# Performance work log

Hardware: AMD Instinct MI355X
Metric: run time of the kernel (lower is better)

The kernel has to match this reference:

```python
import jax, jax.numpy as jnp
import numpy as np

N, E, F, H = 50000, 800000, 64, 4
NEG_SLOPE = 0.2
LN_EPS = 1e-5


def setup_inputs() -> dict:
    key = jax.random.key(0)
    ks = jax.random.split(key, 12)
    h = jax.random.normal(ks[0], (N, F), dtype=jnp.float32)
    src = jax.random.randint(ks[1], (E,), 0, N, dtype=jnp.int32)
    dst = jax.random.randint(ks[2], (E,), 0, N, dtype=jnp.int32)
    s = 1.0 / np.sqrt(F)
    fc_w = jax.random.uniform(ks[3], (F, H * F), jnp.float32, -s, s)
    attn_l = jax.random.normal(ks[4], (H, F), dtype=jnp.float32) * s
    attn_r = jax.random.normal(ks[5], (H, F), dtype=jnp.float32) * s
    gat_bias = jnp.zeros((H * F,), dtype=jnp.float32)
    so = 1.0 / np.sqrt(H * F)
    out_w = jax.random.uniform(ks[6], (H * F, F), jnp.float32, -so, so)
    out_b = jax.random.uniform(ks[7], (F,), jnp.float32, -so, so)
    ln_g = jnp.ones((F,), dtype=jnp.float32)
    ln_b = jnp.zeros((F,), dtype=jnp.float32)
    return {"h": h, "src": src, "dst": dst, "fc_w": fc_w, "attn_l": attn_l,
            "attn_r": attn_r, "gat_bias": gat_bias, "out_w": out_w,
            "out_b": out_b, "ln_g": ln_g, "ln_b": ln_b}


def reference(h, src, dst, fc_w, attn_l, attn_r, gat_bias, out_w, out_b, ln_g, ln_b):
    # --- GATConv (DGL semantics) ---
    feat = (h @ fc_w).reshape(N, H, F)                      # [N,H,F]
    el = jnp.einsum('nhf,hf->nh', feat, attn_l)             # [N,H]
    er = jnp.einsum('nhf,hf->nh', feat, attn_r)             # [N,H]
    e = jax.nn.leaky_relu(el[src] + er[dst], NEG_SLOPE)     # [E,H]
    # edge softmax over incoming edges of each dst node
    m = jax.ops.segment_max(e, dst, num_segments=N)         # [N,H]
    ex = jnp.exp(e - m[dst])                                # [E,H]
    z = jax.ops.segment_sum(ex, dst, num_segments=N)        # [N,H]
    alpha = ex / z[dst]                                     # [E,H]
    msg = feat[src] * alpha[:, :, None]                     # [E,H,F]
    rst = jax.ops.segment_sum(msg, dst, num_segments=N)     # [N,H,F]
    rst = rst + gat_bias.reshape(H, F)
    # --- out linear + layernorm ---
    x = rst.reshape(N, H * F) @ out_w + out_b               # [N,F]
    mu = jnp.mean(x, axis=-1, keepdims=True)
    var = jnp.var(x, axis=-1, keepdims=True)
    return (x - mu) * jax.lax.rsqrt(var + LN_EPS) * ln_g + ln_b
```

## Files before the change

### kernel.cpp

```cpp
#include <hip/hip_runtime.h>

#define NN 50000
#define EE 800000
#define FF 64
#define HH 4
#define HF 256
#define NEG_SLOPE 0.2f
#define LN_EPS 1e-5f
#define WPACK_N (4 * 8 * 64 * 8)
#define WPACKA_N (16 * 2 * 64 * 8)
#define NTILE (NN / 16)
#define TROW 264

typedef __attribute__((ext_vector_type(8))) short s8v;
typedef __attribute__((ext_vector_type(4))) float f4v;

__device__ __forceinline__ unsigned short f32_to_bf16_rne(float x) {
  unsigned int u = __float_as_uint(x);
  unsigned int r = u + 0x7FFFu + ((u >> 16) & 1u);
  return (unsigned short)(r >> 16);
}

__device__ __forceinline__ float readlane_f(float v, int l) {
  return __uint_as_float(
      (unsigned)__builtin_amdgcn_readlane((int)__float_as_uint(v), l));
}

__global__ __launch_bounds__(256) void k_prep(
    const float* __restrict__ fc_w, const float* __restrict__ out_w,
    unsigned short* __restrict__ wpackA, unsigned short* __restrict__ wpack,
    int* __restrict__ cnt) {
  const int idx = blockIdx.x * 256 + threadIdx.x;
  if (idx < WPACKA_N) {
    const int j = idx & 7;
    const int l = (idx >> 3) & 63;
    const int t = (idx >> 9) & 1;
    const int ct = idx >> 10;
    const int k = 32 * t + (l >> 4) * 8 + j;
    const int c = 16 * ct + (l & 15);
    wpackA[idx] = f32_to_bf16_rne(fc_w[k * HF + c]);
  } else if (idx < WPACKA_N + WPACK_N) {
    const int i2 = idx - WPACKA_N;
    const int j = i2 & 7;
    const int l = (i2 >> 3) & 63;
    const int t = (i2 >> 9) & 7;
    const int ct = i2 >> 12;
    const int k = 32 * t + (l >> 4) * 8 + j;
    const int c = 16 * ct + (l & 15);
    wpack[i2] = f32_to_bf16_rne(out_w[k * FF + c]);
  }
  if (idx < NN) cnt[idx] = 0;
}

__global__ __launch_bounds__(256) void k_feat(
    const float* __restrict__ h, const unsigned short* __restrict__ wpackA,
    const float* __restrict__ attn_l, const float* __restrict__ attn_r,
    unsigned short* __restrict__ featb, float* __restrict__ el,
    float* __restrict__ er) {
  __shared__ unsigned short wlds[WPACKA_N];
  {
    const uint4* s = (const uint4*)wpackA;
    uint4* d = (uint4*)wlds;
    for (int i = threadIdx.x; i < 2048; i += 256) d[i] = s[i];
  }
  __syncthreads();
  const int wave = threadIdx.x >> 6;
  const int lane = threadIdx.x & 63;
  const int tile = blockIdx.x * 4 + wave;
  if (tile >= NTILE) return;
  const int n0 = tile * 16;
  const int cl = lane & 15;
  const int quad = lane >> 4;

  float al[16], ar[16];
#pragma unroll
  for (int ct = 0; ct < 16; ++ct) {
    al[ct] = attn_l[16 * ct + cl];
    ar[ct] = attn_r[16 * ct + cl];
  }

  s8v a[2];
#pragma unroll
  for (int t = 0; t < 2; ++t) {
    const float* hp = h + (size_t)(n0 + cl) * FF + 32 * t + quad * 8;
    float hv[8];
    *(float4*)hv = *(const float4*)hp;
    *(float4*)(hv + 4) = *(const float4*)(hp + 4);
    s8v av;
#pragma unroll
    for (int i = 0; i < 8; ++i) av[i] = (short)f32_to_bf16_rne(hv[i]);
    a[t] = av;
  }

  f4v acc[16];
#pragma unroll
  for (int ct = 0; ct < 16; ++ct) {
    f4v z = {0.f, 0.f, 0.f, 0.f};
    acc[ct] = z;
#pragma unroll
    for (int t = 0; t < 2; ++t) {
      const s8v b = *(const s8v*)(wlds + ((ct * 2 + t) * 64 + lane) * 8);
      acc[ct] = __builtin_amdgcn_mfma_f32_16x16x32_bf16(a[t], b, acc[ct], 0, 0, 0);
    }
  }

#pragma unroll
  for (int r = 0; r < 4; ++r) {
    const int n = n0 + quad * 4 + r;
    float pl[4] = {0.f, 0.f, 0.f, 0.f};
    float pr[4] = {0.f, 0.f, 0.f, 0.f};
#pragma unroll
    for (int g = 0; g < 4; ++g) {
      const float x0 = acc[g][r];
      const float x1 = acc[g + 4][r];
      const float x2 = acc[g + 8][r];
      const float x3 = acc[g + 12][r];
      uint2 pk;
      pk.x = (unsigned)f32_to_bf16_rne(x0) | ((unsigned)f32_to_bf16_rne(x1) << 16);
      pk.y = (unsigned)f32_to_bf16_rne(x2) | ((unsigned)f32_to_bf16_rne(x3) << 16);
      *(uint2*)(featb + (size_t)n * HF + (16 * g + cl) * 4) = pk;
      pl[0] = fmaf(x0, al[g], pl[0]);      pr[0] = fmaf(x0, ar[g], pr[0]);
      pl[1] = fmaf(x1, al[g + 4], pl[1]);  pr[1] = fmaf(x1, ar[g + 4], pr[1]);
      pl[2] = fmaf(x2, al[g + 8], pl[2]);  pr[2] = fmaf(x2, ar[g + 8], pr[2]);
      pl[3] = fmaf(x3, al[g + 12], pl[3]); pr[3] = fmaf(x3, ar[g + 12], pr[3]);
    }
#pragma unroll
    for (int off = 1; off < 16; off <<= 1) {
#pragma unroll
      for (int hh = 0; hh < 4; ++hh) {
        pl[hh] += __shfl_xor(pl[hh], off, 64);
        pr[hh] += __shfl_xor(pr[hh], off, 64);
      }
    }
    if (cl == 0) {
      *(float4*)(el + (size_t)n * 4) = make_float4(pl[0], pl[1], pl[2], pl[3]);
      *(float4*)(er + (size_t)n * 4) = make_float4(pr[0], pr[1], pr[2], pr[3]);
    }
  }
}

__global__ void k_scatter(const int* __restrict__ src,
                          const int* __restrict__ dst,
                          int* __restrict__ cnt, int* __restrict__ colp) {
  int e = blockIdx.x * blockDim.x + threadIdx.x;
  if (e < EE) {
    const int d = dst[e];
    const int pos = atomicAdd(&cnt[d], 1);
    if (pos < 64) colp[(d << 6) | pos] = src[e];
  }
}

__global__ __launch_bounds__(256) void k_gather_out(
    const unsigned short* __restrict__ featb, const float* __restrict__ el,
    const float* __restrict__ er, const int* __restrict__ cnt,
    const int* __restrict__ colp, const float* __restrict__ gat_bias,
    const unsigned short* __restrict__ wpack, const float* __restrict__ out_b,
    const float* __restrict__ ln_g, const float* __restrict__ ln_b,
    float* __restrict__ out) {
  __shared__ unsigned short tile[16][TROW];
  const int wave = threadIdx.x >> 6;
  const int lane = threadIdx.x & 63;
  const int n0 = blockIdx.x * 16;
  const float gb0 = gat_bias[lane], gb1 = gat_bias[64 + lane];
  const float gb2 = gat_bias[128 + lane], gb3 = gat_bias[192 + lane];
  const unsigned short* fb = featb + lane * HH;

#pragma unroll
  for (int r = 0; r < 4; ++r) {
    const int row = wave * 4 + r;
    const int n = n0 + row;
    const int m = cnt[n];
    const float4 erv = *(const float4*)(er + (size_t)n * 4);
    float a0 = 0.f, a1 = 0.f, a2 = 0.f, a3 = 0.f;
    float z0 = 0.f, z1 = 0.f, z2 = 0.f, z3 = 0.f;
    float w0 = 0.f, w1 = 0.f, w2 = 0.f, w3 = 0.f;
    int s = 0;
    if (lane < m) {
      s = colp[(n << 6) | lane];
      const float4 elv = *(const float4*)(el + (size_t)s * 4);
      float e0 = elv.x + erv.x, e1 = elv.y + erv.y;
      float e2 = elv.z + erv.z, e3 = elv.w + erv.w;
      e0 = e0 > 0.f ? e0 : NEG_SLOPE * e0;
      e1 = e1 > 0.f ? e1 : NEG_SLOPE * e1;
      e2 = e2 > 0.f ? e2 : NEG_SLOPE * e2;
      e3 = e3 > 0.f ? e3 : NEG_SLOPE * e3;
      w0 = __expf(e0); w1 = __expf(e1);
      w2 = __expf(e2); w3 = __expf(e3);
    }
    for (int e = 0; e < m; e += 8) {
#pragma unroll
      for (int j = 0; j < 8; ++j) {
        const int le = e + j;
        const int se = __builtin_amdgcn_readlane(s, le);
        const float we0 = readlane_f(w0, le);
        const float we1 = readlane_f(w1, le);
        const float we2 = readlane_f(w2, le);
        const float we3 = readlane_f(w3, le);
        const uint2 d = *(const uint2*)(fb + (size_t)se * HF);
        z0 += we0; z1 += we1; z2 += we2; z3 += we3;
        a0 = fmaf(we0, __uint_as_float(d.x << 16), a0);
        a1 = fmaf(we1, __uint_as_float(d.x & 0xFFFF0000u), a1);
        a2 = fmaf(we2, __uint_as_float(d.y << 16), a2);
        a3 = fmaf(we3, __uint_as_float(d.y & 0xFFFF0000u), a3);
      }
    }
    tile[row][lane]       = f32_to_bf16_rne((z0 > 0.f ? a0 / z0 : 0.f) + gb0);
    tile[row][64 + lane]  = f32_to_bf16_rne((z1 > 0.f ? a1 / z1 : 0.f) + gb1);
    tile[row][128 + lane] = f32_to_bf16_rne((z2 > 0.f ? a2 / z2 : 0.f) + gb2);
    tile[row][192 + lane] = f32_to_bf16_rne((z3 > 0.f ? a3 / z3 : 0.f) + gb3);
  }
  __syncthreads();
  if (wave != 0) return;

  const int cl = lane & 15;
  const int quad = lane >> 4;
  s8v a[8];
#pragma unroll
  for (int t = 0; t < 8; ++t)
    a[t] = *(const s8v*)(&tile[cl][32 * t + quad * 8]);

  f4v acc[4];
#pragma unroll
  for (int ct = 0; ct < 4; ++ct) {
    f4v z = {0.f, 0.f, 0.f, 0.f};
    acc[ct] = z;
#pragma unroll
    for (int t = 0; t < 8; ++t) {
      const s8v b = *(const s8v*)(wpack + ((ct * 8 + t) * 64 + lane) * 8);
      acc[ct] = __builtin_amdgcn_mfma_f32_16x16x32_bf16(a[t], b, acc[ct], 0, 0, 0);
    }
  }

  float x[4][4];
  float s1[4], s2[4];
#pragma unroll
  for (int r = 0; r < 4; ++r) { s1[r] = 0.f; s2[r] = 0.f; }
#pragma unroll
  for (int ct = 0; ct < 4; ++ct) {
    const float ob = out_b[16 * ct + cl];
#pragma unroll
    for (int r = 0; r < 4; ++r) {
      const float v = acc[ct][r] + ob;
      x[ct][r] = v;
      s1[r] += v;
      s2[r] += v * v;
    }
  }
#pragma unroll
  for (int r = 0; r < 4; ++r) {
#pragma unroll
    for (int off = 1; off < 16; off <<= 1) {
      s1[r] += __shfl_xor(s1[r], off, 64);
      s2[r] += __shfl_xor(s2[r], off, 64);
    }
  }
#pragma unroll
  for (int r = 0; r < 4; ++r) {
    const float mu = s1[r] * (1.f / 64.f);
    const float var = s2[r] * (1.f / 64.f) - mu * mu;
    const float inv = rsqrtf(var + LN_EPS);
    const int row = n0 + quad * 4 + r;
#pragma unroll
    for (int ct = 0; ct < 4; ++ct) {
      const int c = 16 * ct + cl;
      out[(size_t)row * FF + c] = (x[ct][r] - mu) * inv * ln_g[c] + ln_b[c];
    }
  }
}

extern "C" void kernel_launch(void* const* d_in, const int* in_sizes, int n_in,
                              void* d_out, int out_size, void* d_ws,
                              size_t ws_size, hipStream_t stream) {
  const float* h_in   = (const float*)d_in[0];
  const int*   src    = (const int*)d_in[1];
  const int*   dst    = (const int*)d_in[2];
  const float* fc_w   = (const float*)d_in[3];
  const float* attn_l = (const float*)d_in[4];
  const float* attn_r = (const float*)d_in[5];
  const float* gbias  = (const float*)d_in[6];
  const float* out_w  = (const float*)d_in[7];
  const float* out_b  = (const float*)d_in[8];
  const float* ln_g   = (const float*)d_in[9];
  const float* ln_b   = (const float*)d_in[10];
  float* out = (float*)d_out;

  char* p = (char*)d_ws;
  auto alloc = [&](size_t bytes) {
    char* q = p;
    p += (bytes + 255) & ~(size_t)255;
    return q;
  };
  unsigned short* featb  = (unsigned short*)alloc((size_t)NN * HF * 2);
  unsigned short* wpack  = (unsigned short*)alloc((size_t)WPACK_N * 2);
  unsigned short* wpackA = (unsigned short*)alloc((size_t)WPACKA_N * 2);
  float* el      = (float*)alloc((size_t)NN * HH * 4);
  float* er      = (float*)alloc((size_t)NN * HH * 4);
  int*   cnt     = (int*)alloc((size_t)NN * 4);
  int*   colp    = (int*)alloc((size_t)NN * 64 * 4);

  k_prep<<<256, 256, 0, stream>>>(fc_w, out_w, wpackA, wpack, cnt);
  k_feat<<<(NTILE + 3) / 4, 256, 0, stream>>>(h_in, wpackA, attn_l, attn_r,
                                              featb, el, er);
  k_scatter<<<(EE + 255) / 256, 256, 0, stream>>>(src, dst, cnt, colp);
  k_gather_out<<<NTILE, 256, 0, stream>>>(featb, el, er, cnt, colp, gbias,
                                          wpack, out_b, ln_g, ln_b, out);
}
```

Baseline: 210.2 us.

## Interleave gathers across four rows and split output GEMM over all waves

Each wave now computes edge weights for its four destination rows up front and gets the softmax denominators with a wave-wide shuffle reduction. It then issues the feature gathers for all four rows in one batch per 8-edge step, which raises memory-level parallelism over the old row-by-row loop. The output projection and LayerNorm are split so that each of the four waves computes one 16-column tile, with the row statistics combined through shared memory. The cost is more registers held for the batched gathers, which may lower occupancy, plus an extra barrier.

```diff
diff --git a/kernel.cpp b/kernel.cpp
--- a/kernel.cpp
+++ b/kernel.cpp
@@ -158,24 +158,24 @@
     const float* __restrict__ ln_g, const float* __restrict__ ln_b,
     float* __restrict__ out) {
   __shared__ unsigned short tile[16][TROW];
+  __shared__ float part[4][16][2];
   const int wave = threadIdx.x >> 6;
   const int lane = threadIdx.x & 63;
   const int n0 = blockIdx.x * 16;
-  const float gb0 = gat_bias[lane], gb1 = gat_bias[64 + lane];
-  const float gb2 = gat_bias[128 + lane], gb3 = gat_bias[192 + lane];
   const unsigned short* fb = featb + lane * HH;
 
-#pragma unroll
-  for (int r = 0; r < 4; ++r) {
-    const int row = wave * 4 + r;
-    const int n = n0 + row;
-    const int m = cnt[n];
+  int mr[4], sv[4];
+  float wa[4], wb[4], wc[4], wd[4];
+#pragma unroll
+  for (int r = 0; r < 4; ++r) {
+    const int n = n0 + wave * 4 + r;
+    int m = cnt[n];
+    m = m > 64 ? 64 : m;
+    mr[r] = __builtin_amdgcn_readfirstlane(m);
     const float4 erv = *(const float4*)(er + (size_t)n * 4);
-    float a0 = 0.f, a1 = 0.f, a2 = 0.f, a3 = 0.f;
-    float z0 = 0.f, z1 = 0.f, z2 = 0.f, z3 = 0.f;
-    float w0 = 0.f, w1 = 0.f, w2 = 0.f, w3 = 0.f;
     int s = 0;
-    if (lane < m) {
+    float x0 = 0.f, x1 = 0.f, x2 = 0.f, x3 = 0.f;
+    if (lane < mr[r]) {
       s = colp[(n << 6) | lane];
       const float4 elv = *(const float4*)(el + (size_t)s * 4);
       float e0 = elv.x + erv.x, e1 = elv.y + erv.y;
@@ -184,87 +184,122 @@
       e1 = e1 > 0.f ? e1 : NEG_SLOPE * e1;
       e2 = e2 > 0.f ? e2 : NEG_SLOPE * e2;
       e3 = e3 > 0.f ? e3 : NEG_SLOPE * e3;
-      w0 = __expf(e0); w1 = __expf(e1);
-      w2 = __expf(e2); w3 = __expf(e3);
-    }
-    for (int e = 0; e < m; e += 8) {
-#pragma unroll
-      for (int j = 0; j < 8; ++j) {
-        const int le = e + j;
-        const int se = __builtin_amdgcn_readlane(s, le);
-        const float we0 = readlane_f(w0, le);
-        const float we1 = readlane_f(w1, le);
-        const float we2 = readlane_f(w2, le);
-        const float we3 = readlane_f(w3, le);
-        const uint2 d = *(const uint2*)(fb + (size_t)se * HF);
-        z0 += we0; z1 += we1; z2 += we2; z3 += we3;
-        a0 = fmaf(we0, __uint_as_float(d.x << 16), a0);
-        a1 = fmaf(we1, __uint_as_float(d.x & 0xFFFF0000u), a1);
-        a2 = fmaf(we2, __uint_as_float(d.y << 16), a2);
-        a3 = fmaf(we3, __uint_as_float(d.y & 0xFFFF0000u), a3);
+      x0 = __expf(e0); x1 = __expf(e1);
+      x2 = __expf(e2); x3 = __expf(e3);
+    }
+    sv[r] = s;
+    wa[r] = x0; wb[r] = x1; wc[r] = x2; wd[r] = x3;
+  }
+
+  float za[4], zb[4], zc[4], zd[4];
+#pragma unroll
+  for (int r = 0; r < 4; ++r) {
+    float z0 = wa[r], z1 = wb[r], z2 = wc[r], z3 = wd[r];
+#pragma unroll
+    for (int off = 1; off < 64; off <<= 1) {
+      z0 += __shfl_xor(z0, off, 64);
+      z1 += __shfl_xor(z1, off, 64);
+      z2 += __shfl_xor(z2, off, 64);
+      z3 += __shfl_xor(z3, off, 64);
+    }
+    za[r] = z0; zb[r] = z1; zc[r] = z2; zd[r] = z3;
+  }
+
+  float a0[4] = {0.f, 0.f, 0.f, 0.f};
+  float a1[4] = {0.f, 0.f, 0.f, 0.f};
+  float a2[4] = {0.f, 0.f, 0.f, 0.f};
+  float a3[4] = {0.f, 0.f, 0.f, 0.f};
+  int mmax = mr[0] > mr[1] ? mr[0] : mr[1];
+  mmax = mmax > mr[2] ? mmax : mr[2];
+  mmax = mmax > mr[3] ? mmax : mr[3];
+
+  for (int e = 0; e < mmax; e += 8) {
+    uint2 d[4][8];
+#pragma unroll
+    for (int r = 0; r < 4; ++r) {
+      if (e < mr[r]) {
+#pragma unroll
+        for (int j = 0; j < 8; ++j) {
+          const int se = __builtin_amdgcn_readlane(sv[r], e + j);
+          d[r][j] = *(const uint2*)(fb + (size_t)se * HF);
+        }
       }
     }
-    tile[row][lane]       = f32_to_bf16_rne((z0 > 0.f ? a0 / z0 : 0.f) + gb0);
-    tile[row][64 + lane]  = f32_to_bf16_rne((z1 > 0.f ? a1 / z1 : 0.f) + gb1);
-    tile[row][128 + lane] = f32_to_bf16_rne((z2 > 0.f ? a2 / z2 : 0.f) + gb2);
-    tile[row][192 + lane] = f32_to_bf16_rne((z3 > 0.f ? a3 / z3 : 0.f) + gb3);
+#pragma unroll
+    for (int r = 0; r < 4; ++r) {
+      if (e < mr[r]) {
+#pragma unroll
+        for (int j = 0; j < 8; ++j) {
+          const int le = e + j;
+          const float we0 = readlane_f(wa[r], le);
+          const float we1 = readlane_f(wb[r], le);
+          const float we2 = readlane_f(wc[r], le);
+          const float we3 = readlane_f(wd[r], le);
+          a0[r] = fmaf(we0, __uint_as_float(d[r][j].x << 16), a0[r]);
+          a1[r] = fmaf(we1, __uint_as_float(d[r][j].x & 0xFFFF0000u), a1[r]);
+          a2[r] = fmaf(we2, __uint_as_float(d[r][j].y << 16), a2[r]);
+          a3[r] = fmaf(we3, __uint_as_float(d[r][j].y & 0xFFFF0000u), a3[r]);
+        }
+      }
+    }
+  }
+
+  const float gb0 = gat_bias[lane], gb1 = gat_bias[64 + lane];
+  const float gb2 = gat_bias[128 + lane], gb3 = gat_bias[192 + lane];
+#pragma unroll
+  for (int r = 0; r < 4; ++r) {
+    const int row = wave * 4 + r;
+    tile[row][lane]       = f32_to_bf16_rne((za[r] > 0.f ? a0[r] / za[r] : 0.f) + gb0);
+    tile[row][64 + lane]  = f32_to_bf16_rne((zb[r] > 0.f ? a1[r] / zb[r] : 0.f) + gb1);
+    tile[row][128 + lane] = f32_to_bf16_rne((zc[r] > 0.f ? a2[r] / zc[r] : 0.f) + gb2);
+    tile[row][192 + lane] = f32_to_bf16_rne((zd[r] > 0.f ? a3[r] / zd[r] : 0.f) + gb3);
   }
   __syncthreads();
-  if (wave != 0) return;
 
   const int cl = lane & 15;
   const int quad = lane >> 4;
-  s8v a[8];
+  s8v afr[8];
 #pragma unroll
   for (int t = 0; t < 8; ++t)
-    a[t] = *(const s8v*)(&tile[cl][32 * t + quad * 8]);
-
-  f4v acc[4];
-#pragma unroll
-  for (int ct = 0; ct < 4; ++ct) {
-    f4v z = {0.f, 0.f, 0.f, 0.f};
-    acc[ct] = z;
-#pragma unroll
-    for (int t = 0; t < 8; ++t) {
-      const s8v b = *(const s8v*)(wpack + ((ct * 8 + t) * 64 + lane) * 8);
-      acc[ct] = __builtin_amdgcn_mfma_f32_16x16x32_bf16(a[t], b, acc[ct], 0, 0, 0);
-    }
-  }
-
-  float x[4][4];
-  float s1[4], s2[4];
-#pragma unroll
-  for (int r = 0; r < 4; ++r) { s1[r] = 0.f; s2[r] = 0.f; }
-#pragma unroll
-  for (int ct = 0; ct < 4; ++ct) {
-    const float ob = out_b[16 * ct + cl];
-#pragma unroll
-    for (int r = 0; r < 4; ++r) {
-      const float v = acc[ct][r] + ob;
-      x[ct][r] = v;
-      s1[r] += v;
-      s2[r] += v * v;
-    }
-  }
-#pragma unroll
-  for (int r = 0; r < 4; ++r) {
+    afr[t] = *(const s8v*)(&tile[cl][32 * t + quad * 8]);
+
+  f4v acc = {0.f, 0.f, 0.f, 0.f};
+#pragma unroll
+  for (int t = 0; t < 8; ++t) {
+    const s8v b = *(const s8v*)(wpack + ((wave * 8 + t) * 64 + lane) * 8);
+    acc = __builtin_amdgcn_mfma_f32_16x16x32_bf16(afr[t], b, acc, 0, 0, 0);
+  }
+
+  const float ob = out_b[16 * wave + cl];
+  float xv[4];
+#pragma unroll
+  for (int r = 0; r < 4; ++r) {
+    const float v = acc[r] + ob;
+    xv[r] = v;
+    float p1 = v, p2 = v * v;
 #pragma unroll
     for (int off = 1; off < 16; off <<= 1) {
-      s1[r] += __shfl_xor(s1[r], off, 64);
-      s2[r] += __shfl_xor(s2[r], off, 64);
-    }
-  }
-#pragma unroll
-  for (int r = 0; r < 4; ++r) {
-    const float mu = s1[r] * (1.f / 64.f);
-    const float var = s2[r] * (1.f / 64.f) - mu * mu;
+      p1 += __shfl_xor(p1, off, 64);
+      p2 += __shfl_xor(p2, off, 64);
+    }
+    if (cl == 0) {
+      part[wave][quad * 4 + r][0] = p1;
+      part[wave][quad * 4 + r][1] = p2;
+    }
+  }
+  __syncthreads();
+#pragma unroll
+  for (int r = 0; r < 4; ++r) {
+    const int row = quad * 4 + r;
+    const float t1 = part[0][row][0] + part[1][row][0] +
+                     part[2][row][0] + part[3][row][0];
+    const float t2 = part[0][row][1] + part[1][row][1] +
+                     part[2][row][1] + part[3][row][1];
+    const float mu = t1 * (1.f / 64.f);
+    const float var = t2 * (1.f / 64.f) - mu * mu;
     const float inv = rsqrtf(var + LN_EPS);
-    const int row = n0 + quad * 4 + r;
-#pragma unroll
-    for (int ct = 0; ct < 4; ++ct) {
-      const int c = 16 * ct + cl;
-      out[(size_t)row * FF + c] = (x[ct][r] - mu) * inv * ln_g[c] + ln_b[c];
-    }
+    const int c = 16 * wave + cl;
+    out[(size_t)(n0 + row) * FF + c] = (xv[r] - mu) * inv * ln_g[c] + ln_b[c];
   }
 }
 
```

After: 236.4 us. 12.5% more time.

## Fuse edge scatter and feature projection into one horizontally-fused kernel

Applied to the files above, without the earlier changes.

Merges the CSR-bucket scatter kernel and the feature-projection MFMA kernel into a single launch, with block ranges split between the two independent jobs so they can run concurrently and one launch gap disappears. The feature path also stops staging the packed weights in LDS and reads B fragments straight from global memory (L2/L1-cached), so there is no block-level sync. The trade-off is more global loads per wave for the weights and a possible loss of occupancy balance, since the scatter blocks are light and the feat blocks are heavy.

```diff
diff --git a/kernel.cpp b/kernel.cpp
--- a/kernel.cpp
+++ b/kernel.cpp
@@ -11,6 +11,8 @@
 #define WPACKA_N (16 * 2 * 64 * 8)
 #define NTILE (NN / 16)
 #define TROW 264
+#define FEAT_BLOCKS ((NTILE + 3) / 4)
+#define SCAT_BLOCKS ((EE + 255) / 256)
 
 typedef __attribute__((ext_vector_type(8))) short s8v;
 typedef __attribute__((ext_vector_type(4))) float f4v;
@@ -52,21 +54,27 @@
   if (idx < NN) cnt[idx] = 0;
 }
 
-__global__ __launch_bounds__(256) void k_feat(
+__global__ __launch_bounds__(256) void k_feat_scatter(
     const float* __restrict__ h, const unsigned short* __restrict__ wpackA,
     const float* __restrict__ attn_l, const float* __restrict__ attn_r,
     unsigned short* __restrict__ featb, float* __restrict__ el,
-    float* __restrict__ er) {
-  __shared__ unsigned short wlds[WPACKA_N];
-  {
-    const uint4* s = (const uint4*)wpackA;
-    uint4* d = (uint4*)wlds;
-    for (int i = threadIdx.x; i < 2048; i += 256) d[i] = s[i];
-  }
-  __syncthreads();
+    float* __restrict__ er, const int* __restrict__ src,
+    const int* __restrict__ dst, int* __restrict__ cnt,
+    int* __restrict__ colp) {
+  const int bid = blockIdx.x;
+  if (bid < SCAT_BLOCKS) {
+    const int e = bid * 256 + threadIdx.x;
+    if (e < EE) {
+      const int sv = src[e];
+      const int d = dst[e];
+      const int pos = atomicAdd(&cnt[d], 1);
+      if (pos < 64) colp[(d << 6) | pos] = sv;
+    }
+    return;
+  }
   const int wave = threadIdx.x >> 6;
   const int lane = threadIdx.x & 63;
-  const int tile = blockIdx.x * 4 + wave;
+  const int tile = (bid - SCAT_BLOCKS) * 4 + wave;
   if (tile >= NTILE) return;
   const int n0 = tile * 16;
   const int cl = lane & 15;
@@ -99,7 +107,7 @@
     acc[ct] = z;
 #pragma unroll
     for (int t = 0; t < 2; ++t) {
-      const s8v b = *(const s8v*)(wlds + ((ct * 2 + t) * 64 + lane) * 8);
+      const s8v b = *(const s8v*)(wpackA + ((ct * 2 + t) * 64 + lane) * 8);
       acc[ct] = __builtin_amdgcn_mfma_f32_16x16x32_bf16(a[t], b, acc[ct], 0, 0, 0);
     }
   }
@@ -136,17 +144,6 @@
       *(float4*)(el + (size_t)n * 4) = make_float4(pl[0], pl[1], pl[2], pl[3]);
       *(float4*)(er + (size_t)n * 4) = make_float4(pr[0], pr[1], pr[2], pr[3]);
     }
-  }
-}
-
-__global__ void k_scatter(const int* __restrict__ src,
-                          const int* __restrict__ dst,
-                          int* __restrict__ cnt, int* __restrict__ colp) {
-  int e = blockIdx.x * blockDim.x + threadIdx.x;
-  if (e < EE) {
-    const int d = dst[e];
-    const int pos = atomicAdd(&cnt[d], 1);
-    if (pos < 64) colp[(d << 6) | pos] = src[e];
   }
 }
 
@@ -299,9 +296,8 @@
   int*   colp    = (int*)alloc((size_t)NN * 64 * 4);
 
   k_prep<<<256, 256, 0, stream>>>(fc_w, out_w, wpackA, wpack, cnt);
-  k_feat<<<(NTILE + 3) / 4, 256, 0, stream>>>(h_in, wpackA, attn_l, attn_r,
-                                              featb, el, er);
-  k_scatter<<<(EE + 255) / 256, 256, 0, stream>>>(src, dst, cnt, colp);
+  k_feat_scatter<<<SCAT_BLOCKS + FEAT_BLOCKS, 256, 0, stream>>>(
+      h_in, wpackA, attn_l, attn_r, featb, el, er, src, dst, cnt, colp);
   k_gather_out<<<NTILE, 256, 0, stream>>>(featb, el, er, cnt, colp, gbias,
                                           wpack, out_b, ln_g, ln_b, out);
 }
```

Result: slower. 226.1 us (+7.6%).

## Fold fc_w into out_w and attention vectors; aggregate raw h instead of feat

Applied to the files above, without the earlier changes.

Uses linearity to precompute fc_w·out_w per head, fc_w·attn_l/attn_r, and gat_bias·out_w+out_b in the prep kernel. The per-node projection to the 256-wide feat tensor is removed: el/er come from dot products of h with the folded vectors, and the gather aggregates 64-wide bf16 h rows with per-head weights. This cuts gather traffic from 512 B to 128 B per edge and eliminates the feat GEMM. The attention weights are normalised once up front instead of dividing after accumulation. Rounding changes because the folded weights are quantised to bf16 and h is rounded to bf16 before aggregation.

```diff
diff --git a/kernel.cpp b/kernel.cpp
--- a/kernel.cpp
+++ b/kernel.cpp
@@ -8,7 +8,6 @@
 #define NEG_SLOPE 0.2f
 #define LN_EPS 1e-5f
 #define WPACK_N (4 * 8 * 64 * 8)
-#define WPACKA_N (16 * 2 * 64 * 8)
 #define NTILE (NN / 16)
 #define TROW 264
 
@@ -28,113 +27,73 @@
 
 __global__ __launch_bounds__(256) void k_prep(
     const float* __restrict__ fc_w, const float* __restrict__ out_w,
-    unsigned short* __restrict__ wpackA, unsigned short* __restrict__ wpack,
+    const float* __restrict__ attn_l, const float* __restrict__ attn_r,
+    const float* __restrict__ gat_bias, const float* __restrict__ out_b,
+    unsigned short* __restrict__ wpack, float* __restrict__ alv,
+    float* __restrict__ arv, float* __restrict__ outb2,
     int* __restrict__ cnt) {
   const int idx = blockIdx.x * 256 + threadIdx.x;
-  if (idx < WPACKA_N) {
+  if (idx < WPACK_N) {
     const int j = idx & 7;
     const int l = (idx >> 3) & 63;
-    const int t = (idx >> 9) & 1;
-    const int ct = idx >> 10;
+    const int t = (idx >> 9) & 7;
+    const int ct = idx >> 12;
     const int k = 32 * t + (l >> 4) * 8 + j;
     const int c = 16 * ct + (l & 15);
-    wpackA[idx] = f32_to_bf16_rne(fc_w[k * HF + c]);
-  } else if (idx < WPACKA_N + WPACK_N) {
-    const int i2 = idx - WPACKA_N;
-    const int j = i2 & 7;
-    const int l = (i2 >> 3) & 63;
-    const int t = (i2 >> 9) & 7;
-    const int ct = i2 >> 12;
-    const int k = 32 * t + (l >> 4) * 8 + j;
-    const int c = 16 * ct + (l & 15);
-    wpack[i2] = f32_to_bf16_rne(out_w[k * FF + c]);
+    const int hh = k >> 6, kk = k & 63;
+    const float* fw = fc_w + kk * HF + hh * FF;
+    const float* ow = out_w + (size_t)(hh * FF) * FF + c;
+    float acc = 0.f;
+#pragma unroll
+    for (int ff = 0; ff < FF; ++ff) acc = fmaf(fw[ff], ow[(size_t)ff * FF], acc);
+    wpack[idx] = f32_to_bf16_rne(acc);
+  } else if (idx < WPACK_N + 512) {
+    const int i = idx - WPACK_N;
+    const int hh = (i >> 6) & 3, kk = i & 63;
+    const float* fw = fc_w + kk * HF + hh * FF;
+    const float* at = (i < 256 ? attn_l : attn_r) + hh * FF;
+    float acc = 0.f;
+#pragma unroll
+    for (int ff = 0; ff < FF; ++ff) acc = fmaf(fw[ff], at[ff], acc);
+    (i < 256 ? alv : arv)[(hh << 6) | kk] = acc;
+  } else if (idx < WPACK_N + 512 + FF) {
+    const int c = idx - WPACK_N - 512;
+    float acc = out_b[c];
+    for (int k = 0; k < HF; ++k) acc = fmaf(gat_bias[k], out_w[(size_t)k * FF + c], acc);
+    outb2[c] = acc;
   }
   if (idx < NN) cnt[idx] = 0;
 }
 
-__global__ __launch_bounds__(256) void k_feat(
-    const float* __restrict__ h, const unsigned short* __restrict__ wpackA,
-    const float* __restrict__ attn_l, const float* __restrict__ attn_r,
-    unsigned short* __restrict__ featb, float* __restrict__ el,
-    float* __restrict__ er) {
-  __shared__ unsigned short wlds[WPACKA_N];
-  {
-    const uint4* s = (const uint4*)wpackA;
-    uint4* d = (uint4*)wlds;
-    for (int i = threadIdx.x; i < 2048; i += 256) d[i] = s[i];
-  }
-  __syncthreads();
+__global__ __launch_bounds__(256) void k_elr(
+    const float* __restrict__ h, const float* __restrict__ alv,
+    const float* __restrict__ arv, unsigned short* __restrict__ hb,
+    float* __restrict__ el, float* __restrict__ er) {
   const int wave = threadIdx.x >> 6;
   const int lane = threadIdx.x & 63;
-  const int tile = blockIdx.x * 4 + wave;
-  if (tile >= NTILE) return;
-  const int n0 = tile * 16;
-  const int cl = lane & 15;
-  const int quad = lane >> 4;
-
-  float al[16], ar[16];
-#pragma unroll
-  for (int ct = 0; ct < 16; ++ct) {
-    al[ct] = attn_l[16 * ct + cl];
-    ar[ct] = attn_r[16 * ct + cl];
-  }
-
-  s8v a[2];
-#pragma unroll
-  for (int t = 0; t < 2; ++t) {
-    const float* hp = h + (size_t)(n0 + cl) * FF + 32 * t + quad * 8;
-    float hv[8];
-    *(float4*)hv = *(const float4*)hp;
-    *(float4*)(hv + 4) = *(const float4*)(hp + 4);
-    s8v av;
-#pragma unroll
-    for (int i = 0; i < 8; ++i) av[i] = (short)f32_to_bf16_rne(hv[i]);
-    a[t] = av;
-  }
-
-  f4v acc[16];
-#pragma unroll
-  for (int ct = 0; ct < 16; ++ct) {
-    f4v z = {0.f, 0.f, 0.f, 0.f};
-    acc[ct] = z;
-#pragma unroll
-    for (int t = 0; t < 2; ++t) {
-      const s8v b = *(const s8v*)(wlds + ((ct * 2 + t) * 64 + lane) * 8);
-      acc[ct] = __builtin_amdgcn_mfma_f32_16x16x32_bf16(a[t], b, acc[ct], 0, 0, 0);
-    }
-  }
-
-#pragma unroll
-  for (int r = 0; r < 4; ++r) {
-    const int n = n0 + quad * 4 + r;
-    float pl[4] = {0.f, 0.f, 0.f, 0.f};
-    float pr[4] = {0.f, 0.f, 0.f, 0.f};
-#pragma unroll
-    for (int g = 0; g < 4; ++g) {
-      const float x0 = acc[g][r];
-      const float x1 = acc[g + 4][r];
-      const float x2 = acc[g + 8][r];
-      const float x3 = acc[g + 12][r];
-      uint2 pk;
-      pk.x = (unsigned)f32_to_bf16_rne(x0) | ((unsigned)f32_to_bf16_rne(x1) << 16);
-      pk.y = (unsigned)f32_to_bf16_rne(x2) | ((unsigned)f32_to_bf16_rne(x3) << 16);
-      *(uint2*)(featb + (size_t)n * HF + (16 * g + cl) * 4) = pk;
-      pl[0] = fmaf(x0, al[g], pl[0]);      pr[0] = fmaf(x0, ar[g], pr[0]);
-      pl[1] = fmaf(x1, al[g + 4], pl[1]);  pr[1] = fmaf(x1, ar[g + 4], pr[1]);
-      pl[2] = fmaf(x2, al[g + 8], pl[2]);  pr[2] = fmaf(x2, ar[g + 8], pr[2]);
-      pl[3] = fmaf(x3, al[g + 12], pl[3]); pr[3] = fmaf(x3, ar[g + 12], pr[3]);
-    }
-#pragma unroll
-    for (int off = 1; off < 16; off <<= 1) {
-#pragma unroll
-      for (int hh = 0; hh < 4; ++hh) {
-        pl[hh] += __shfl_xor(pl[hh], off, 64);
-        pr[hh] += __shfl_xor(pr[hh], off, 64);
-      }
-    }
-    if (cl == 0) {
-      *(float4*)(el + (size_t)n * 4) = make_float4(pl[0], pl[1], pl[2], pl[3]);
-      *(float4*)(er + (size_t)n * 4) = make_float4(pr[0], pr[1], pr[2], pr[3]);
+  const int n0 = blockIdx.x * 16 + wave * 4;
+  float av[4], bv[4];
+#pragma unroll
+  for (int hh = 0; hh < 4; ++hh) {
+    av[hh] = alv[(hh << 6) | lane];
+    bv[hh] = arv[(hh << 6) | lane];
+  }
+#pragma unroll
+  for (int r = 0; r < 4; ++r) {
+    const int n = n0 + r;
+    const float hv = h[(size_t)n * FF + lane];
+    hb[(size_t)n * FF + lane] = f32_to_bf16_rne(hv);
+    float p[8];
+#pragma unroll
+    for (int hh = 0; hh < 4; ++hh) { p[hh] = hv * av[hh]; p[4 + hh] = hv * bv[hh]; }
+#pragma unroll
+    for (int off = 1; off < 64; off <<= 1) {
+#pragma unroll
+      for (int q = 0; q < 8; ++q) p[q] += __shfl_xor(p[q], off, 64);
+    }
+    if (lane == 0) {
+      *(float4*)(el + (size_t)n * 4) = make_float4(p[0], p[1], p[2], p[3]);
+      *(float4*)(er + (size_t)n * 4) = make_float4(p[4], p[5], p[6], p[7]);
     }
   }
 }
@@ -151,19 +110,17 @@
 }
 
 __global__ __launch_bounds__(256) void k_gather_out(
-    const unsigned short* __restrict__ featb, const float* __restrict__ el,
+    const unsigned short* __restrict__ hb, const float* __restrict__ el,
     const float* __restrict__ er, const int* __restrict__ cnt,
-    const int* __restrict__ colp, const float* __restrict__ gat_bias,
-    const unsigned short* __restrict__ wpack, const float* __restrict__ out_b,
+    const int* __restrict__ colp,
+    const unsigned short* __restrict__ wpack, const float* __restrict__ outb2,
     const float* __restrict__ ln_g, const float* __restrict__ ln_b,
     float* __restrict__ out) {
   __shared__ unsigned short tile[16][TROW];
   const int wave = threadIdx.x >> 6;
   const int lane = threadIdx.x & 63;
   const int n0 = blockIdx.x * 16;
-  const float gb0 = gat_bias[lane], gb1 = gat_bias[64 + lane];
-  const float gb2 = gat_bias[128 + lane], gb3 = gat_bias[192 + lane];
-  const unsigned short* fb = featb + lane * HH;
+  const unsigned short* fb = hb + lane;
 
 #pragma unroll
   for (int r = 0; r < 4; ++r) {
@@ -171,10 +128,8 @@
     const int n = n0 + row;
     const int m = cnt[n];
     const float4 erv = *(const float4*)(er + (size_t)n * 4);
-    float a0 = 0.f, a1 = 0.f, a2 = 0.f, a3 = 0.f;
-    float z0 = 0.f, z1 = 0.f, z2 = 0.f, z3 = 0.f;
+    int s = 0;
     float w0 = 0.f, w1 = 0.f, w2 = 0.f, w3 = 0.f;
-    int s = 0;
     if (lane < m) {
       s = colp[(n << 6) | lane];
       const float4 elv = *(const float4*)(el + (size_t)s * 4);
@@ -187,27 +142,41 @@
       w0 = __expf(e0); w1 = __expf(e1);
       w2 = __expf(e2); w3 = __expf(e3);
     }
+    float z0 = w0, z1 = w1, z2 = w2, z3 = w3;
+#pragma unroll
+    for (int off = 1; off < 64; off <<= 1) {
+      z0 += __shfl_xor(z0, off, 64);
+      z1 += __shfl_xor(z1, off, 64);
+      z2 += __shfl_xor(z2, off, 64);
+      z3 += __shfl_xor(z3, off, 64);
+    }
+    w0 *= (z0 > 0.f ? 1.f / z0 : 0.f);
+    w1 *= (z1 > 0.f ? 1.f / z1 : 0.f);
+    w2 *= (z2 > 0.f ? 1.f / z2 : 0.f);
+    w3 *= (z3 > 0.f ? 1.f / z3 : 0.f);
+
+    float a0 = 0.f, a1 = 0.f, a2 = 0.f, a3 = 0.f;
     for (int e = 0; e < m; e += 8) {
 #pragma unroll
       for (int j = 0; j < 8; ++j) {
         const int le = e + j;
         const int se = __builtin_amdgcn_readlane(s, le);
+        const float xv = __uint_as_float(
+            (unsigned)fb[(size_t)se * FF] << 16);
         const float we0 = readlane_f(w0, le);
         const float we1 = readlane_f(w1, le);
         const float we2 = readlane_f(w2, le);
         const float we3 = readlane_f(w3, le);
-        const uint2 d = *(const uint2*)(fb + (size_t)se * HF);
-        z0 += we0; z1 += we1; z2 += we2; z3 += we3;
-        a0 = fmaf(we0, __uint_as_float(d.x << 16), a0);
-        a1 = fmaf(we1, __uint_as_float(d.x & 0xFFFF0000u), a1);
-        a2 = fmaf(we2, __uint_as_float(d.y << 16), a2);
-        a3 = fmaf(we3, __uint_as_float(d.y & 0xFFFF0000u), a3);
+        a0 = fmaf(we0, xv, a0);
+        a1 = fmaf(we1, xv, a1);
+        a2 = fmaf(we2, xv, a2);
+        a3 = fmaf(we3, xv, a3);
       }
     }
-    tile[row][lane]       = f32_to_bf16_rne((z0 > 0.f ? a0 / z0 : 0.f) + gb0);
-    tile[row][64 + lane]  = f32_to_bf16_rne((z1 > 0.f ? a1 / z1 : 0.f) + gb1);
-    tile[row][128 + lane] = f32_to_bf16_rne((z2 > 0.f ? a2 / z2 : 0.f) + gb2);
-    tile[row][192 + lane] = f32_to_bf16_rne((z3 > 0.f ? a3 / z3 : 0.f) + gb3);
+    tile[row][lane]       = f32_to_bf16_rne(a0);
+    tile[row][64 + lane]  = f32_to_bf16_rne(a1);
+    tile[row][128 + lane] = f32_to_bf16_rne(a2);
+    tile[row][192 + lane] = f32_to_bf16_rne(a3);
   }
   __syncthreads();
   if (wave != 0) return;
@@ -237,7 +206,7 @@
   for (int r = 0; r < 4; ++r) { s1[r] = 0.f; s2[r] = 0.f; }
 #pragma unroll
   for (int ct = 0; ct < 4; ++ct) {
-    const float ob = out_b[16 * ct + cl];
+    const float ob = outb2[16 * ct + cl];
 #pragma unroll
     for (int r = 0; r < 4; ++r) {
       const float v = acc[ct][r] + ob;
@@ -290,18 +259,20 @@
     p += (bytes + 255) & ~(size_t)255;
     return q;
   };
-  unsigned short* featb  = (unsigned short*)alloc((size_t)NN * HF * 2);
+  unsigned short* hb     = (unsigned short*)alloc((size_t)NN * FF * 2);
   unsigned short* wpack  = (unsigned short*)alloc((size_t)WPACK_N * 2);
-  unsigned short* wpackA = (unsigned short*)alloc((size_t)WPACKA_N * 2);
+  float* alv     = (float*)alloc(256 * 4);
+  float* arv     = (float*)alloc(256 * 4);
+  float* outb2   = (float*)alloc(64 * 4);
   float* el      = (float*)alloc((size_t)NN * HH * 4);
   float* er      = (float*)alloc((size_t)NN * HH * 4);
   int*   cnt     = (int*)alloc((size_t)NN * 4);
   int*   colp    = (int*)alloc((size_t)NN * 64 * 4);
 
-  k_prep<<<256, 256, 0, stream>>>(fc_w, out_w, wpackA, wpack, cnt);
-  k_feat<<<(NTILE + 3) / 4, 256, 0, stream>>>(h_in, wpackA, attn_l, attn_r,
-                                              featb, el, er);
+  k_prep<<<256, 256, 0, stream>>>(fc_w, out_w, attn_l, attn_r, gbias, out_b,
+                                  wpack, alv, arv, outb2, cnt);
+  k_elr<<<NTILE, 256, 0, stream>>>(h_in, alv, arv, hb, el, er);
   k_scatter<<<(EE + 255) / 256, 256, 0, stream>>>(src, dst, cnt, colp);
-  k_gather_out<<<NTILE, 256, 0, stream>>>(featb, el, er, cnt, colp, gbias,
-                                          wpack, out_b, ln_g, ln_b, out);
-}
+  k_gather_out<<<NTILE, 256, 0, stream>>>(hb, el, er, cnt, colp, wpack,
+                                          outb2, ln_g, ln_b, out);
+}
```

New measurement: 217.9 us. 3.7% more time.
